# Kernel optimization log

Hardware: AMD Instinct MI355X
Metric: run time of the kernel (lower is better)

## Reference

```python
import jax, jax.numpy as jnp
import numpy as np

B_, L_ = 8, 2048            # batch, seq_len
AD, VD, H = 512, 512, 256    # audio_dim, visual_dim, hidden_dim (= mamba d_model)
EXPAND, DSTATE, DCONV = 2, 16, 4
DIN = EXPAND * H             # mamba d_inner = 512
DTRANK = (H + 15) // 16      # ceil(d_model/16) = 16
NCLS = 8


def setup_inputs() -> dict:
    key = jax.random.key(0)
    ks = jax.random.split(key, 16)
    w = lambda k, shape, s=0.02: jax.random.normal(k, shape, jnp.float32) * s
    return {
        "audio_feats": jax.random.normal(ks[0], (B_, L_, AD), jnp.float32),
        "visual_feats": jax.random.normal(ks[1], (B_, L_, VD), jnp.float32),
        "audio_w": w(ks[2], (H, AD)), "audio_b": jnp.zeros((H,), jnp.float32),
        "visual_w": w(ks[3], (H, VD)), "visual_b": jnp.zeros((H,), jnp.float32),
        "q_w": w(ks[4], (H, H)), "q_b": jnp.zeros((H,), jnp.float32),
        "k_w": w(ks[5], (H, H)), "k_b": jnp.zeros((H,), jnp.float32),
        "v_w": w(ks[6], (H, H)), "v_b": jnp.zeros((H,), jnp.float32),
        "in_proj_w": w(ks[7], (2 * DIN, H)),
        "conv_w": w(ks[8], (DIN, DCONV), 0.1), "conv_b": jnp.zeros((DIN,), jnp.float32),
        "x_proj_w": w(ks[9], (DTRANK + 2 * DSTATE, DIN)),
        "dt_proj_w": w(ks[10], (DIN, DTRANK), 0.1),
        "dt_proj_b": jnp.full((DIN,), -4.0, jnp.float32),  # softplus(-4) ~ small dt
        "A_log": jnp.log(jnp.tile(jnp.arange(1, DSTATE + 1, dtype=jnp.float32), (DIN, 1))),
        "D": jnp.ones((DIN,), jnp.float32),
        "out_proj_w": w(ks[11], (H, DIN)),
        "cls_w": w(ks[12], (NCLS, H)), "cls_b": jnp.zeros((NCLS,), jnp.float32),
    }


def _linear(x, w, b):
    return jnp.einsum('...i,oi->...o', x, w) + b


def _mamba(u, in_proj_w, conv_w, conv_b, x_proj_w, dt_proj_w, dt_proj_b, A_log, D, out_proj_w):
    # u: [B, L, d_model]
    xz = jnp.einsum('bld,ed->ble', u, in_proj_w)          # [B, L, 2*DIN]
    x, z = jnp.split(xz, 2, axis=-1)
    # causal depthwise conv1d (torch pads d_conv-1 both sides then truncates to L)
    lhs = jnp.swapaxes(x, 1, 2)                            # [B, DIN, L]
    rhs = conv_w[:, None, :]                               # [DIN, 1, DCONV]
    xc = jax.lax.conv_general_dilated(lhs, rhs, (1,), [(DCONV - 1, 0)],
                                      feature_group_count=DIN)
    x = jax.nn.silu(jnp.swapaxes(xc, 1, 2) + conv_b)       # [B, L, DIN]
    dbc = jnp.einsum('bld,ed->ble', x, x_proj_w)           # [B, L, DTRANK+2*DSTATE]
    dt, Bm, Cm = jnp.split(dbc, [DTRANK, DTRANK + DSTATE], axis=-1)
    dt = jax.nn.softplus(jnp.einsum('blr,dr->bld', dt, dt_proj_w) + dt_proj_b)
    A = -jnp.exp(A_log)                                    # [DIN, DSTATE]

    def step(h, inputs):
        dt_t, B_t, C_t, x_t = inputs                       # [B,DIN],[B,DSTATE],[B,DSTATE],[B,DIN]
        dA = jnp.exp(dt_t[:, :, None] * A)                 # [B, DIN, DSTATE]
        h = dA * h + (dt_t * x_t)[:, :, None] * B_t[:, None, :]
        y = jnp.einsum('bds,bs->bd', h, C_t)
        return h, y

    h0 = jnp.zeros((u.shape[0], DIN, DSTATE), x.dtype)
    xs = (jnp.swapaxes(dt, 0, 1), jnp.swapaxes(Bm, 0, 1),
          jnp.swapaxes(Cm, 0, 1), jnp.swapaxes(x, 0, 1))
    _, ys = jax.lax.scan(step, h0, xs)                     # ys: [L, B, DIN]
    y = jnp.swapaxes(ys, 0, 1) + x * D
    y = y * jax.nn.silu(z)
    return jnp.einsum('bld,od->blo', y, out_proj_w)        # [B, L, d_model]


def reference(audio_feats, visual_feats, audio_w, audio_b, visual_w, visual_b,
              q_w, q_b, k_w, k_b, v_w, v_b, in_proj_w, conv_w, conv_b,
              x_proj_w, dt_proj_w, dt_proj_b, A_log, D, out_proj_w, cls_w, cls_b):
    ah = _linear(audio_feats, audio_w, audio_b)            # [B, L, H]
    vh = _linear(visual_feats, visual_w, visual_b)         # [B, L, H]
    Q = _linear(ah, q_w, q_b)
    K = _linear(vh, k_w, k_b)
    V = _linear(vh, v_w, v_b)
    scores = jnp.einsum('bqd,bkd->bqk', Q, K) / jnp.sqrt(jnp.float32(H))
    attn = jax.nn.softmax(scores, axis=-1)                 # [B, L, L]
    fused = jnp.einsum('bqk,bkd->bqd', attn, V)            # [B, L, H]
    mo = _mamba(fused, in_proj_w, conv_w, conv_b, x_proj_w,
                dt_proj_w, dt_proj_b, A_log, D, out_proj_w)
    pooled = mo.mean(axis=1)                               # [B, H]
    logits = _linear(pooled, cls_w, cls_b)                 # [B, NCLS]
    preds = jax.nn.softmax(logits, axis=-1)
    return logits, preds
```

## Files before the change

kernel.cpp:

```cpp
#include <hip/hip_runtime.h>
#include <hip/hip_bf16.h>
#include <math.h>

#define B_    8
#define L_    2048
#define AD    512
#define VD    512
#define H_    256
#define DIN   512
#define DSTATE 16
#define DCONV  4
#define DTRANK 16
#define NCLS   8
#define BL    (B_ * L_)
#define NCH   64
#define CLEN  32
#define NSP   4
#define NGRP  8

typedef __attribute__((ext_vector_type(8))) short bf16x8;
typedef __attribute__((ext_vector_type(4))) float f32x4;

__device__ inline bf16x8 pack8(float4 a, float4 b)
{
    bf16x8 o; __hip_bfloat16 t;
    t = __float2bfloat16(a.x); o[0] = *(short*)&t;
    t = __float2bfloat16(a.y); o[1] = *(short*)&t;
    t = __float2bfloat16(a.z); o[2] = *(short*)&t;
    t = __float2bfloat16(a.w); o[3] = *(short*)&t;
    t = __float2bfloat16(b.x); o[4] = *(short*)&t;
    t = __float2bfloat16(b.y); o[5] = *(short*)&t;
    t = __float2bfloat16(b.z); o[6] = *(short*)&t;
    t = __float2bfloat16(b.w); o[7] = *(short*)&t;
    return o;
}

__device__ __forceinline__ void gload_lds16(const void* g, void* l)
{
    __builtin_amdgcn_global_load_lds(
        (const __attribute__((address_space(1))) void*)g,
        (__attribute__((address_space(3))) void*)l,
        16, 0, 0);
}

__global__ __launch_bounds__(256)
void cast_inputs_kernel(const float* __restrict__ a, const float* __restrict__ v,
                        __hip_bfloat16* __restrict__ ab, __hip_bfloat16* __restrict__ vb)
{
    size_t i = ((size_t)blockIdx.x * 256 + threadIdx.x) * 8;
    const float* s; __hip_bfloat16* d; size_t off;
    if (i < 8388608) { s = a; d = ab; off = i; }
    else             { s = v; d = vb; off = i - 8388608; }
    float4 x = *(const float4*)(s + off);
    float4 y = *(const float4*)(s + off + 4);
    *(bf16x8*)(d + off) = pack8(x, y);
}

__global__ __launch_bounds__(256)
void prep_kernel(const float* __restrict__ qw, const float* __restrict__ kw,
                 const float* __restrict__ vw, const float* __restrict__ ipw,
                 const float* __restrict__ xpw,
                 const float* __restrict__ aw, const float* __restrict__ vww,
                 const float* __restrict__ ab, const float* __restrict__ vb,
                 const float* __restrict__ qb, const float* __restrict__ kb,
                 const float* __restrict__ vb2,
                 __hip_bfloat16* __restrict__ qwb, __hip_bfloat16* __restrict__ kwb,
                 __hip_bfloat16* __restrict__ vwb, __hip_bfloat16* __restrict__ ipwb,
                 __hip_bfloat16* __restrict__ xpwb,
                 __hip_bfloat16* __restrict__ awT, __hip_bfloat16* __restrict__ vwT,
                 float* __restrict__ bq, float* __restrict__ bkv)
{
    const int blk = blockIdx.x;
    if (blk < 236) {
        size_t i = ((size_t)blk * 256 + threadIdx.x) * 8;
        const float* s; __hip_bfloat16* d; size_t off;
        if      (i <  65536) { s = qw;  d = qwb;  off = i; }
        else if (i < 131072) { s = kw;  d = kwb;  off = i - 65536; }
        else if (i < 196608) { s = vw;  d = vwb;  off = i - 131072; }
        else if (i < 458752) { s = ipw; d = ipwb; off = i - 196608; }
        else                 { s = xpw; d = xpwb; off = i - 458752; }
        float4 x = *(const float4*)(s + off);
        float4 y = *(const float4*)(s + off + 4);
        *(bf16x8*)(d + off) = pack8(x, y);
    } else if (blk < 1260) {
        int i = (blk - 236) * 256 + threadIdx.x;
        const float* s = (i < 131072) ? aw : vww;
        __hip_bfloat16* d = (i < 131072) ? awT : vwT;
        int j = i & 131071;
        int r = j >> 9, c = j & 511;
        d[c * 256 + r] = __float2bfloat16(s[j]);
    } else {
        int seg = blk - 1260;
        int m = threadIdx.x;
        const float* w  = (seg == 0) ? qw : (seg == 1) ? kw : vw;
        const float* ib = (seg == 0) ? ab : vb;
        const float* ob = (seg == 0) ? qb : (seg == 1) ? kb : vb2;
        float s = ob[m];
        for (int i = 0; i < 256; ++i) s += w[m * 256 + i] * ib[i];
        if (seg == 0) bq[m] = s;
        else          bkv[(seg - 1) * 256 + m] = s;
    }
}

__global__ __launch_bounds__(64, 2)
void gemm_comp_kernel(const __hip_bfloat16* __restrict__ qw,
                      const __hip_bfloat16* __restrict__ kw,
                      const __hip_bfloat16* __restrict__ vw,
                      const __hip_bfloat16* __restrict__ awT,
                      const __hip_bfloat16* __restrict__ vwT,
                      __hip_bfloat16* __restrict__ Wqp,
                      __hip_bfloat16* __restrict__ Wkvp)
{
    const int seg = blockIdx.z;
    const __hip_bfloat16* A = (seg == 0) ? qw : (seg == 1) ? kw : vw;
    const __hip_bfloat16* W = (seg == 0) ? awT : vwT;
    __hip_bfloat16* outp = (seg == 0) ? Wqp : (Wkvp + (size_t)(seg - 1) * 256 * 512);

    const int lane = threadIdx.x;
    const int l15  = lane & 15;
    const int quad = lane >> 4;
    const int m0   = blockIdx.x * 16;
    const int n0   = blockIdx.y * 64;

    const __hip_bfloat16* Arow = A + (size_t)(m0 + l15) * 256 + quad * 8;
    f32x4 acc[4];
    #pragma unroll
    for (int nt = 0; nt < 4; ++nt) acc[nt] = (f32x4){0.f, 0.f, 0.f, 0.f};

    #pragma unroll
    for (int kc = 0; kc < 256; kc += 32) {
        bf16x8 af = *(const bf16x8*)(Arow + kc);
        #pragma unroll
        for (int nt = 0; nt < 4; ++nt) {
            bf16x8 bfv = *(const bf16x8*)(W + (size_t)(n0 + nt * 16 + l15) * 256 + kc + quad * 8);
            acc[nt] = __builtin_amdgcn_mfma_f32_16x16x32_bf16(af, bfv, acc[nt], 0, 0, 0);
        }
    }
    #pragma unroll
    for (int nt = 0; nt < 4; ++nt) {
        int col = n0 + nt * 16 + l15;
        #pragma unroll
        for (int r = 0; r < 4; ++r)
            outp[(size_t)(m0 + quad * 4 + r) * 512 + col] = __float2bfloat16(acc[nt][r]);
    }
}

template<int N, int K, int NT, int OBF, int ACT>
__global__ __launch_bounds__(256, 2)
void gemm4_t(const __hip_bfloat16* __restrict__ A,
             const __hip_bfloat16* __restrict__ W,
             const float* __restrict__ bias,
             void* __restrict__ outp)
{
    constexpr int NROWS = NT * 16;
    __shared__ __attribute__((aligned(16))) short Ws[NROWS * 264];
    const int tid  = threadIdx.x;
    const int lane = tid & 63;
    const int w    = tid >> 6;
    const int l15  = lane & 15;
    const int quad = lane >> 4;
    const int m0   = blockIdx.x * 64 + w * 16;
    const int n0   = blockIdx.y * 64;

    constexpr int KC = K / 32;
    bf16x8 af[KC];
    const __hip_bfloat16* Arow = A + (size_t)(m0 + l15) * K + quad * 8;
    #pragma unroll
    for (int kc = 0; kc < KC; ++kc) af[kc] = *(const bf16x8*)(Arow + kc * 32);

    f32x4 acc[NT];
    #pragma unroll
    for (int nt = 0; nt < NT; ++nt) acc[nt] = (f32x4){0.f, 0.f, 0.f, 0.f};

    #pragma unroll
    for (int kh = 0; kh < K / 256; ++kh) {
        __syncthreads();
        #pragma unroll
        for (int i = 0; i < 8; ++i) {
            int id = tid + i * 256;
            int row = id >> 5, c = id & 31;
            if (row < NROWS)
                *(bf16x8*)&Ws[row * 264 + c * 8] =
                    *(const bf16x8*)(W + (size_t)(n0 + row) * K + kh * 256 + c * 8);
        }
        __syncthreads();
        #pragma unroll
        for (int kc = 0; kc < 8; ++kc) {
            #pragma unroll
            for (int nt = 0; nt < NT; ++nt) {
                bf16x8 wv = *(const bf16x8*)&Ws[(nt * 16 + l15) * 264 + kc * 32 + quad * 8];
                acc[nt] = __builtin_amdgcn_mfma_f32_16x16x32_bf16(af[kh * 8 + kc], wv, acc[nt], 0, 0, 0);
            }
        }
    }
    #pragma unroll
    for (int nt = 0; nt < NT; ++nt) {
        int col = n0 + nt * 16 + l15;
        float bv = bias ? bias[col] : 0.f;
        #pragma unroll
        for (int r = 0; r < 4; ++r) {
            size_t idx = (size_t)(m0 + quad * 4 + r) * N + col;
            float v = acc[nt][r] + bv;
            if (ACT) v = v / (1.f + __expf(-v));
            if (OBF) ((__hip_bfloat16*)outp)[idx] = __float2bfloat16(v);
            else     ((float*)outp)[idx] = v;
        }
    }
}

__global__ __launch_bounds__(256)
void transpose_v_kernel(const __hip_bfloat16* __restrict__ KV,
                        __hip_bfloat16* __restrict__ Vt)
{
    const int tid = threadIdx.x;
    const int lc  = blockIdx.x & 7;
    const int hg  = (blockIdx.x >> 3) & 31;
    const int b   = blockIdx.x >> 8;
    const int l   = lc * 256 + tid;
    bf16x8 v = *(const bf16x8*)(KV + ((size_t)b * L_ + l) * 512 + 256 + hg * 8);
    __hip_bfloat16* dst = Vt + (size_t)b * H_ * L_ + (size_t)(hg * 8) * L_ + l;
    #pragma unroll
    for (int j = 0; j < 8; ++j) {
        short s = v[j];
        dst[(size_t)j * L_] = *(__hip_bfloat16*)&s;
    }
}

__global__ __launch_bounds__(256, 2)
void attn_split_kernel(const __hip_bfloat16* __restrict__ Q,
                       const __hip_bfloat16* __restrict__ KV,
                       const __hip_bfloat16* __restrict__ Vt,
                       __hip_bfloat16* __restrict__ Opart,
                       float* __restrict__ lpart)
{
    __shared__ __attribute__((aligned(16))) short Ks[2][32 * 256];
    __shared__ __attribute__((aligned(16))) short Vs[2][256 * 32];
    __shared__ __attribute__((aligned(16))) short Pls[4][2][16 * 40];

    const int tid  = threadIdx.x;
    const int lane = tid & 63;
    const int w    = tid >> 6;
    const int b    = blockIdx.x & 7;
    const int qt   = (blockIdx.x >> 3) & 15;
    const int sp   = blockIdx.x >> 7;
    const int q0   = qt * 128 + w * 32;
    const int l15  = lane & 15;
    const int quad = lane >> 4;
    const int wb   = tid & 192;

    const __hip_bfloat16* Qb = Q  + ((size_t)b * L_ + q0) * H_;
    const __hip_bfloat16* Kb = KV + (size_t)b * L_ * 512;
    const __hip_bfloat16* Vb = Vt + (size_t)b * H_ * L_;

    bf16x8 qf[2][8];
    #pragma unroll
    for (int s2 = 0; s2 < 2; ++s2)
        #pragma unroll
        for (int kc = 0; kc < 8; ++kc)
            qf[s2][kc] = *(const bf16x8*)(Qb + (size_t)(s2 * 16 + l15) * H_ + kc * 32 + quad * 8);

    f32x4 Oacc[2][16];
    #pragma unroll
    for (int s2 = 0; s2 < 2; ++s2)
        #pragma unroll
        for (int nt = 0; nt < 16; ++nt) Oacc[s2][nt] = (f32x4){0.f, 0.f, 0.f, 0.f};
    float lsum[2][4] = {{0.f,0.f,0.f,0.f},{0.f,0.f,0.f,0.f}};

    const int kbase = sp * 512;
    const int sK = l15 & 7;
    const int vcol8 = (quad ^ (l15 & 3)) * 8;

#define STAGE(KsD, VsD, stv) do {                                                 \
        const int kb_ = kbase + (stv) * 32;                                       \
        _Pragma("unroll")                                                         \
        for (int i_ = 0; i_ < 4; ++i_) {                                          \
            int q_ = i_ * 256 + tid;                                              \
            int rK_ = q_ >> 5, cK_ = q_ & 31;                                     \
            gload_lds16(Kb + (size_t)(kb_ + rK_) * 512 + ((cK_ ^ (rK_ & 7)) << 3),\
                        (KsD) + (i_ * 256 + wb) * 8);                             \
            int rV_ = q_ >> 2, cV_ = q_ & 3;                                      \
            gload_lds16(Vb + (size_t)rV_ * L_ + kb_ + ((cV_ ^ (rV_ & 3)) << 3),   \
                        (VsD) + (i_ * 256 + wb) * 8);                             \
        }                                                                         \
    } while (0)

    STAGE(Ks[0], Vs[0], 0);
    __syncthreads();
    for (int st = 0; st < 16; ++st) {
        const int cur = st & 1;
        short* KsC = Ks[cur];
        short* VsC = Vs[cur];
        if (st < 15) STAGE(Ks[cur ^ 1], Vs[cur ^ 1], st + 1);
        #pragma unroll
        for (int nt = 0; nt < 2; ++nt) {
            f32x4 S0 = (f32x4){0.f,0.f,0.f,0.f};
            f32x4 S1 = (f32x4){0.f,0.f,0.f,0.f};
            __builtin_amdgcn_s_setprio(1);
            #pragma unroll
            for (int kc = 0; kc < 8; ++kc) {
                bf16x8 bk = *(const bf16x8*)&KsC[(nt * 16 + l15) * 256 + (((kc * 4 + quad) ^ sK) << 3)];
                S0 = __builtin_amdgcn_mfma_f32_16x16x32_bf16(qf[0][kc], bk, S0, 0, 0, 0);
                S1 = __builtin_amdgcn_mfma_f32_16x16x32_bf16(qf[1][kc], bk, S1, 0, 0, 0);
            }
            __builtin_amdgcn_s_setprio(0);
            #pragma unroll
            for (int r = 0; r < 4; ++r) {
                float p0 = __expf(S0[r] * 0.0625f);
                float p1 = __expf(S1[r] * 0.0625f);
                lsum[0][r] += p0;
                lsum[1][r] += p1;
                __hip_bfloat16 pb0 = __float2bfloat16(p0);
                __hip_bfloat16 pb1 = __float2bfloat16(p1);
                Pls[w][0][(quad * 4 + r) * 40 + nt * 16 + l15] = *(short*)&pb0;
                Pls[w][1][(quad * 4 + r) * 40 + nt * 16 + l15] = *(short*)&pb1;
            }
        }
        bf16x8 pf0 = *(const bf16x8*)&Pls[w][0][l15 * 40 + quad * 8];
        bf16x8 pf1 = *(const bf16x8*)&Pls[w][1][l15 * 40 + quad * 8];
        __builtin_amdgcn_s_setprio(1);
        #pragma unroll
        for (int nt = 0; nt < 16; ++nt) {
            bf16x8 vf = *(const bf16x8*)&VsC[(nt * 16 + l15) * 32 + vcol8];
            Oacc[0][nt] = __builtin_amdgcn_mfma_f32_16x16x32_bf16(pf0, vf, Oacc[0][nt], 0, 0, 0);
            Oacc[1][nt] = __builtin_amdgcn_mfma_f32_16x16x32_bf16(pf1, vf, Oacc[1][nt], 0, 0, 0);
        }
        __builtin_amdgcn_s_setprio(0);
        __syncthreads();
    }
#undef STAGE
    #pragma unroll
    for (int s2 = 0; s2 < 2; ++s2)
        #pragma unroll
        for (int r = 0; r < 4; ++r) {
            lsum[s2][r] += __shfl_xor(lsum[s2][r], 1, 64);
            lsum[s2][r] += __shfl_xor(lsum[s2][r], 2, 64);
            lsum[s2][r] += __shfl_xor(lsum[s2][r], 4, 64);
            lsum[s2][r] += __shfl_xor(lsum[s2][r], 8, 64);
        }
    __hip_bfloat16* Ob = Opart + (((size_t)sp * B_ + b) * L_ + q0) * H_;
    #pragma unroll
    for (int s2 = 0; s2 < 2; ++s2)
        #pragma unroll
        for (int r = 0; r < 4; ++r)
            #pragma unroll
            for (int nt = 0; nt < 16; ++nt)
                Ob[(size_t)(s2 * 16 + quad * 4 + r) * H_ + nt * 16 + l15] =
                    __float2bfloat16(Oacc[s2][nt][r]);
    if (l15 == 0) {
        #pragma unroll
        for (int s2 = 0; s2 < 2; ++s2)
            #pragma unroll
            for (int r = 0; r < 4; ++r)
                lpart[((size_t)sp * B_ + b) * L_ + q0 + s2 * 16 + quad * 4 + r] = lsum[s2][r];
    }
}

__global__ __launch_bounds__(256)
void attn_merge_kernel(const __hip_bfloat16* __restrict__ Opart,
                       const float* __restrict__ lpart,
                       __hip_bfloat16* __restrict__ O)
{
    const size_t i8  = ((size_t)blockIdx.x * 256 + threadIdx.x) * 8;
    const size_t row = i8 >> 8;
    float l = 0.f;
    #pragma unroll
    for (int sp = 0; sp < NSP; ++sp) l += lpart[(size_t)sp * BL + row];
    const float inv = 1.f / l;
    float o[8] = {0.f,0.f,0.f,0.f,0.f,0.f,0.f,0.f};
    #pragma unroll
    for (int sp = 0; sp < NSP; ++sp) {
        bf16x8 v = *(const bf16x8*)(Opart + (size_t)sp * BL * H_ + i8);
        #pragma unroll
        for (int j = 0; j < 8; ++j) {
            short s = v[j];
            o[j] += __bfloat162float(*(__hip_bfloat16*)&s);
        }
    }
    bf16x8 ov;
    #pragma unroll
    for (int j = 0; j < 8; ++j) {
        __hip_bfloat16 t = __float2bfloat16(o[j] * inv);
        ov[j] = *(short*)&t;
    }
    *(bf16x8*)(O + i8) = ov;
}

__global__ __launch_bounds__(256)
void conv_silu_kernel(const __hip_bfloat16* __restrict__ xb,
                      const float* __restrict__ cw,
                      const float* __restrict__ cb,
                      __hip_bfloat16* __restrict__ xconvbf)
{
    const int idx = blockIdx.x * 256 + threadIdx.x;
    const int d0 = (idx & 63) << 3;
    const int l  = (idx >> 6) & (L_ - 1);
    const int b  = idx >> 17;

    float4 wv[8];
    float acc[8];
    #pragma unroll
    for (int j = 0; j < 8; ++j) {
        wv[j]  = *(const float4*)(cw + (d0 + j) * DCONV);
        acc[j] = cb[d0 + j];
    }
    #pragma unroll
    for (int t = 0; t < DCONV; ++t) {
        int ls = l - (DCONV - 1) + t;
        if (ls >= 0) {
            bf16x8 x = *(const bf16x8*)(xb + ((size_t)b * L_ + ls) * DIN + d0);
            #pragma unroll
            for (int j = 0; j < 8; ++j) {
                short s = x[j];
                float xv = __bfloat162float(*(__hip_bfloat16*)&s);
                float wt = (t == 0) ? wv[j].x : (t == 1) ? wv[j].y : (t == 2) ? wv[j].z : wv[j].w;
                acc[j] += xv * wt;
            }
        }
    }
    bf16x8 ov;
    #pragma unroll
    for (int j = 0; j < 8; ++j) {
        float v = acc[j] / (1.f + __expf(-acc[j]));
        __hip_bfloat16 t = __float2bfloat16(v);
        ov[j] = *(short*)&t;
    }
    *(bf16x8*)(xconvbf + (size_t)idx * 8) = ov;
}

__global__ __launch_bounds__(256)
void scan_p1_kernel(const __hip_bfloat16* __restrict__ xconv,
                    const __hip_bfloat16* __restrict__ zw,
                    const float* __restrict__ dbc,
                    const float* __restrict__ dtw,
                    const float* __restrict__ dtbias,
                    const float* __restrict__ A_log,
                    const float* __restrict__ Dv,
                    float* __restrict__ hend,
                    float* __restrict__ aprod,
                    float* __restrict__ Gbuf,
                    float* __restrict__ accloc)
{
    __shared__ float Ds[CLEN][16];
    __shared__ float Bs[CLEN][16];
    __shared__ float Cs[CLEN][16];
    const int tid  = threadIdx.x;
    const int dgrp = blockIdx.x & 1;
    const int c    = (blockIdx.x >> 1) & 63;
    const int b    = blockIdx.x >> 7;
    const int d    = dgrp * 256 + tid;
    const size_t rbase = (size_t)b * L_ + c * CLEN;

    for (int i = tid; i < CLEN * 16; i += 256) {
        int tl = i >> 4, s = i & 15;
        Ds[tl][s] = dbc[(rbase + tl) * 48 + s];
        Bs[tl][s] = dbc[(rbase + tl) * 48 + 16 + s];
        Cs[tl][s] = dbc[(rbase + tl) * 48 + 32 + s];
    }
    __syncthreads();

    float wr[16];
    #pragma unroll
    for (int r = 0; r < 16; ++r) wr[r] = dtw[d * DTRANK + r];
    const float dbias = dtbias[d];
    const float Dval  = Dv[d];

    float Aa[16];
    bool fast = true;
    #pragma unroll
    for (int s = 0; s < 16; ++s) {
        Aa[s] = -__expf(A_log[d * DSTATE + s]);
        fast = fast && (fabsf(Aa[s] + (float)(s + 1)) < 1e-3f);
    }

    float h[16], ap[16], g[16];
    #pragma unroll
    for (int s = 0; s < 16; ++s) { h[s] = 0.f; ap[s] = 1.f; g[s] = 0.f; }
    float acc = 0.f;

    if (fast) {
        for (int t = 0; t < CLEN; ++t) {
            float d0 = dbias, d1 = 0.f;
            #pragma unroll
            for (int r = 0; r < 8; ++r) { d0 += Ds[t][r] * wr[r]; d1 += Ds[t][r + 8] * wr[r + 8]; }
            float dot = d0 + d1;
            float dtv = (dot > 20.f) ? dot : __logf(1.f + __expf(dot));
            float xv  = __bfloat162float(xconv[(rbase + t) * DIN + d]);
            float wt  = __bfloat162float(zw   [(rbase + t) * DIN + d]);
            float u  = dtv * xv;
            float e1 = __expf(-dtv);
            float ep = 1.f;
            #pragma unroll
            for (int s = 0; s < 16; ++s) {
                ep *= e1;
                ap[s] *= ep;
                h[s] = ep * h[s] + u * Bs[t][s];
                float tc = wt * Cs[t][s];
                acc += tc * h[s];
                g[s] += tc * ap[s];
            }
            acc += wt * xv * Dval;
        }
    } else {
        for (int t = 0; t < CLEN; ++t) {
            float d0 = dbias, d1 = 0.f;
            #pragma unroll
            for (int r = 0; r < 8; ++r) { d0 += Ds[t][r] * wr[r]; d1 += Ds[t][r + 8] * wr[r + 8]; }
            float dot = d0 + d1;
            float dtv = (dot > 20.f) ? dot : __logf(1.f + __expf(dot));
            float xv  = __bfloat162float(xconv[(rbase + t) * DIN + d]);
            float wt  = __bfloat162float(zw   [(rbase + t) * DIN + d]);
            float u  = dtv * xv;
            #pragma unroll
            for (int s = 0; s < 16; ++s) {
                float e = __expf(dtv * Aa[s]);
                ap[s] *= e;
                h[s] = e * h[s] + u * Bs[t][s];
                float tc = wt * Cs[t][s];
                acc += tc * h[s];
                g[s] += tc * ap[s];
            }
            acc += wt * xv * Dval;
        }
    }
    size_t o = (((size_t)b * NCH + c) * DIN + d) * 16;
    #pragma unroll
    for (int s = 0; s < 16; ++s) { hend[o + s] = h[s]; aprod[o + s] = ap[s]; Gbuf[o + s] = g[s]; }
    accloc[((size_t)b * NCH + c) * DIN + d] = acc;
}

__global__ __launch_bounds__(256)
void scan_p2a_kernel(const float* __restrict__ hend,
                     const float* __restrict__ aprod,
                     const float* __restrict__ Gbuf,
                     const float* __restrict__ accloc,
                     float* __restrict__ hg, float* __restrict__ Pg,
                     float* __restrict__ Wg, float* __restrict__ part0g,
                     float* __restrict__ accg)
{
    const int g   = blockIdx.x * 256 + threadIdx.x;
    const int b   = g >> 16;
    const int grp = (g >> 13) & 7;
    const int ds  = g & 8191;
    float h = 0.f, P = 1.f, W = 0.f, p0 = 0.f;
    #pragma unroll
    for (int j = 0; j < 8; ++j) {
        int c = grp * 8 + j;
        size_t idx = (((size_t)b * NCH + c) << 13) + ds;
        float G = Gbuf[idx], ap = aprod[idx], he = hend[idx];
        p0 += G * h;
        W  += G * P;
        h   = ap * h + he;
        P  *= ap;
    }
    size_t o = (((size_t)b * NGRP + grp) << 13) + ds;
    hg[o] = h; Pg[o] = P; Wg[o] = W; part0g[o] = p0;
    if (ds < DIN) {
        float a = 0.f;
        #pragma unroll
        for (int j = 0; j < 8; ++j)
            a += accloc[((size_t)b * NCH + grp * 8 + j) * DIN + ds];
        accg[((size_t)b * NGRP + grp) * DIN + ds] = a;
    }
}

__global__ __launch_bounds__(256)
void scan_p2b_kernel(const float* __restrict__ hg, const float* __restrict__ Pg,
                     const float* __restrict__ Wg, const float* __restrict__ part0g,
                     const float* __restrict__ accg,
                     float* __restrict__ ybar)
{
    const int g  = blockIdx.x * 256 + threadIdx.x;
    const int b  = g >> 13;
    const int ds = g & 8191;
    const int d  = ds >> 4;
    const int s  = ds & 15;
    float h = 0.f, part = 0.f;
    #pragma unroll
    for (int grp = 0; grp < NGRP; ++grp) {
        size_t o = (((size_t)b * NGRP + grp) << 13) + ds;
        part += part0g[o] + Wg[o] * h;
        h = Pg[o] * h + hg[o];
    }
    part += __shfl_xor(part, 1, 64);
    part += __shfl_xor(part, 2, 64);
    part += __shfl_xor(part, 4, 64);
    part += __shfl_xor(part, 8, 64);
    if (s == 0) {
        float a = 0.f;
        #pragma unroll
        for (int grp = 0; grp < NGRP; ++grp)
            a += accg[((size_t)b * NGRP + grp) * DIN + d];
        ybar[b * DIN + d] = (part + a) * (1.f / (float)L_);
    }
}

__global__ __launch_bounds__(256)
void head_kernel(const float* __restrict__ ybar,
                 const float* __restrict__ opw,
                 const float* __restrict__ clsw,
                 const float* __restrict__ clsb,
                 float* __restrict__ out)
{
    __shared__ float pooled_s[H_];
    __shared__ float logit_s[NCLS];
    const int tid = threadIdx.x;
    const int b   = blockIdx.x;
    const float* yb = ybar + b * DIN;
    const float* wr = opw + (size_t)tid * DIN;
    float p = 0.f;
    for (int dd = 0; dd < DIN; dd += 4) {
        float4 y4 = *(const float4*)(yb + dd);
        float4 w4 = *(const float4*)(wr + dd);
        p += y4.x*w4.x + y4.y*w4.y + y4.z*w4.z + y4.w*w4.w;
    }
    pooled_s[tid] = p;
    __syncthreads();
    if (tid < NCLS) {
        float lg = clsb[tid];
        const float* cw = clsw + tid * H_;
        for (int hh = 0; hh < H_; ++hh) lg += pooled_s[hh] * cw[hh];
        logit_s[tid] = lg;
        out[b * NCLS + tid] = lg;
    }
    __syncthreads();
    if (tid == 0) {
        float mx = logit_s[0];
        for (int c = 1; c < NCLS; ++c) mx = fmaxf(mx, logit_s[c]);
        float ssum = 0.f; float e[NCLS];
        for (int c = 0; c < NCLS; ++c) { e[c] = __expf(logit_s[c] - mx); ssum += e[c]; }
        for (int c = 0; c < NCLS; ++c) out[B_*NCLS + b * NCLS + c] = e[c] / ssum;
    }
}

extern "C" void kernel_launch(void* const* d_in, const int* in_sizes, int n_in,
                              void* d_out, int out_size, void* d_ws, size_t ws_size,
                              hipStream_t stream)
{
    const float* audio    = (const float*)d_in[0];
    const float* visual   = (const float*)d_in[1];
    const float* audio_w  = (const float*)d_in[2];
    const float* audio_b  = (const float*)d_in[3];
    const float* visual_w = (const float*)d_in[4];
    const float* visual_b = (const float*)d_in[5];
    const float* q_w = (const float*)d_in[6];
    const float* q_b = (const float*)d_in[7];
    const float* k_w = (const float*)d_in[8];
    const float* k_b = (const float*)d_in[9];
    const float* v_w = (const float*)d_in[10];
    const float* v_b = (const float*)d_in[11];
    const float* in_proj_w = (const float*)d_in[12];
    const float* conv_w    = (const float*)d_in[13];
    const float* conv_b    = (const float*)d_in[14];
    const float* x_proj_w  = (const float*)d_in[15];
    const float* dt_proj_w = (const float*)d_in[16];
    const float* dt_proj_b = (const float*)d_in[17];
    const float* A_log     = (const float*)d_in[18];
    const float* Dvec      = (const float*)d_in[19];
    const float* out_proj_w= (const float*)d_in[20];
    const float* cls_w     = (const float*)d_in[21];
    const float* cls_b     = (const float*)d_in[22];
    float* out = (float*)d_out;
    float* ws  = (float*)d_ws;

    __hip_bfloat16* abf  = (__hip_bfloat16*)(ws);
    __hip_bfloat16* vbf  = (__hip_bfloat16*)(ws + 4194304);
    __hip_bfloat16* Qbf  = (__hip_bfloat16*)(ws + 8388608);
    __hip_bfloat16* KVbf = (__hip_bfloat16*)(ws + 10485760);
    __hip_bfloat16* Vt   = (__hip_bfloat16*)(ws + 14680064);
    __hip_bfloat16* fusedbf = (__hip_bfloat16*)(ws + 16777216);
    __hip_bfloat16* Opart   = (__hip_bfloat16*)(ws + 18874368);
    __hip_bfloat16* xconvbf = (__hip_bfloat16*)(ws + 27262976);
    __hip_bfloat16* xbufbf = (__hip_bfloat16*)(ws);
    __hip_bfloat16* zwbf   = (__hip_bfloat16*)(ws + 4194304);
    float* hend   = ws;
    float* Gbuf   = ws + 18874368;
    float* aprod  = ws + 23068672;
    float* hg     = ws + 16777216;
    float* Pg     = ws + 17301504;
    float* Wgb    = ws + 17825792;
    float* part0g = ws + 18350080;
    __hip_bfloat16* q_wbf   = (__hip_bfloat16*)(ws + 31457280);
    __hip_bfloat16* k_wbf   = (__hip_bfloat16*)(ws + 31490048);
    __hip_bfloat16* v_wbf   = (__hip_bfloat16*)(ws + 31522816);
    __hip_bfloat16* ipwbf   = (__hip_bfloat16*)(ws + 31555584);
    __hip_bfloat16* xpwbf   = (__hip_bfloat16*)(ws + 31686656);
    __hip_bfloat16* awT     = (__hip_bfloat16*)(ws + 31698944);
    __hip_bfloat16* vwT     = (__hip_bfloat16*)(ws + 31764480);
    __hip_bfloat16* Wqp     = (__hip_bfloat16*)(ws + 31830016);
    __hip_bfloat16* Wkvp    = (__hip_bfloat16*)(ws + 31895552);
    float* bq     = ws + 32026624;
    float* bkv    = ws + 32026880;
    float* lpart  = ws + 32027392;
    float* dbcb   = ws + 32092928;
    float* accloc = ws + 32879360;
    float* accg   = ws + 33141504;
    float* ybar   = ws + 33174272;
    (void)ws_size;

    dim3 blk(256);
    cast_inputs_kernel<<<dim3(8192), blk, 0, stream>>>(audio, visual, abf, vbf);
    prep_kernel<<<dim3(1263), blk, 0, stream>>>(q_w, k_w, v_w, in_proj_w, x_proj_w,
                                                audio_w, visual_w, audio_b, visual_b,
                                                q_b, k_b, v_b,
                                                q_wbf, k_wbf, v_wbf, ipwbf, xpwbf,
                                                awT, vwT, bq, bkv);
    gemm_comp_kernel<<<dim3(16, 8, 3), dim3(64), 0, stream>>>(q_wbf, k_wbf, v_wbf, awT, vwT, Wqp, Wkvp);
    gemm4_t<256, 512, 4, 1, 0><<<dim3(256, 4), blk, 0, stream>>>(abf, Wqp,  bq,  Qbf);
    gemm4_t<512, 512, 4, 1, 0><<<dim3(256, 8), blk, 0, stream>>>(vbf, Wkvp, bkv, KVbf);
    transpose_v_kernel<<<dim3(2048), blk, 0, stream>>>(KVbf, Vt);
    attn_split_kernel<<<dim3(512), blk, 0, stream>>>(Qbf, KVbf, Vt, Opart, lpart);
    attn_merge_kernel<<<dim3(2048), blk, 0, stream>>>(Opart, lpart, fusedbf);
    gemm4_t<512, 256, 4, 1, 0><<<dim3(256, 8), blk, 0, stream>>>(fusedbf, ipwbf,           nullptr, xbufbf);
    gemm4_t<512, 256, 4, 1, 1><<<dim3(256, 8), blk, 0, stream>>>(fusedbf, ipwbf + DIN*H_,  nullptr, zwbf);
    conv_silu_kernel<<<dim3(4096), blk, 0, stream>>>(xbufbf, conv_w, conv_b, xconvbf);
    gemm4_t<48, 512, 3, 0, 0><<<dim3(256, 1), blk, 0, stream>>>(xconvbf, xpwbf, nullptr, dbcb);
    scan_p1_kernel<<<dim3(1024), blk, 0, stream>>>(xconvbf, zwbf, dbcb, dt_proj_w, dt_proj_b,
                                                   A_log, Dvec, hend, aprod, Gbuf, accloc);
    scan_p2a_kernel<<<dim3(2048), blk, 0, stream>>>(hend, aprod, Gbuf, accloc,
                                                    hg, Pg, Wgb, part0g, accg);
    scan_p2b_kernel<<<dim3(256), blk, 0, stream>>>(hg, Pg, Wgb, part0g, accg, ybar);
    head_kernel<<<dim3(8), blk, 0, stream>>>(ybar, out_proj_w, cls_w, cls_b, out);
}
```

Before: 428.1 us.

## Halve scan chunk length and recompute chunk decay from summed dt

```diff
diff --git a/kernel.cpp b/kernel.cpp
--- a/kernel.cpp
+++ b/kernel.cpp
@@ -13,8 +13,8 @@
 #define DTRANK 16
 #define NCLS   8
 #define BL    (B_ * L_)
-#define NCH   64
-#define CLEN  32
+#define NCH   128
+#define CLEN  16
 #define NSP   4
 #define NGRP  8
 
@@ -436,7 +436,7 @@
                     const float* __restrict__ A_log,
                     const float* __restrict__ Dv,
                     float* __restrict__ hend,
-                    float* __restrict__ aprod,
+                    float* __restrict__ sumdt,
                     float* __restrict__ Gbuf,
                     float* __restrict__ accloc)
 {
@@ -445,8 +445,8 @@
     __shared__ float Cs[CLEN][16];
     const int tid  = threadIdx.x;
     const int dgrp = blockIdx.x & 1;
-    const int c    = (blockIdx.x >> 1) & 63;
-    const int b    = blockIdx.x >> 7;
+    const int c    = (blockIdx.x >> 1) & (NCH - 1);
+    const int b    = blockIdx.x >> 8;
     const int d    = dgrp * 256 + tid;
     const size_t rbase = (size_t)b * L_ + c * CLEN;
 
@@ -476,6 +476,7 @@
     #pragma unroll
     for (int s = 0; s < 16; ++s) { h[s] = 0.f; ap[s] = 1.f; g[s] = 0.f; }
     float acc = 0.f;
+    float dts = 0.f;
 
     if (fast) {
         for (int t = 0; t < CLEN; ++t) {
@@ -489,6 +490,7 @@
             float u  = dtv * xv;
             float e1 = __expf(-dtv);
             float ep = 1.f;
+            dts += dtv;
             #pragma unroll
             for (int s = 0; s < 16; ++s) {
                 ep *= e1;
@@ -510,6 +512,7 @@
             float xv  = __bfloat162float(xconv[(rbase + t) * DIN + d]);
             float wt  = __bfloat162float(zw   [(rbase + t) * DIN + d]);
             float u  = dtv * xv;
+            dts += dtv;
             #pragma unroll
             for (int s = 0; s < 16; ++s) {
                 float e = __expf(dtv * Aa[s]);
@@ -524,15 +527,17 @@
     }
     size_t o = (((size_t)b * NCH + c) * DIN + d) * 16;
     #pragma unroll
-    for (int s = 0; s < 16; ++s) { hend[o + s] = h[s]; aprod[o + s] = ap[s]; Gbuf[o + s] = g[s]; }
+    for (int s = 0; s < 16; ++s) { hend[o + s] = h[s]; Gbuf[o + s] = g[s]; }
+    sumdt [((size_t)b * NCH + c) * DIN + d] = dts;
     accloc[((size_t)b * NCH + c) * DIN + d] = acc;
 }
 
 __global__ __launch_bounds__(256)
 void scan_p2a_kernel(const float* __restrict__ hend,
-                     const float* __restrict__ aprod,
+                     const float* __restrict__ sumdt,
                      const float* __restrict__ Gbuf,
                      const float* __restrict__ accloc,
+                     const float* __restrict__ A_log,
                      float* __restrict__ hg, float* __restrict__ Pg,
                      float* __restrict__ Wg, float* __restrict__ part0g,
                      float* __restrict__ accg)
@@ -541,12 +546,17 @@
     const int b   = g >> 16;
     const int grp = (g >> 13) & 7;
     const int ds  = g & 8191;
+    const int d   = ds >> 4;
+    const int s   = ds & 15;
+    const float Aa = -__expf(A_log[d * DSTATE + s]);
     float h = 0.f, P = 1.f, W = 0.f, p0 = 0.f;
     #pragma unroll
-    for (int j = 0; j < 8; ++j) {
-        int c = grp * 8 + j;
+    for (int j = 0; j < NCH / NGRP; ++j) {
+        int c = grp * (NCH / NGRP) + j;
         size_t idx = (((size_t)b * NCH + c) << 13) + ds;
-        float G = Gbuf[idx], ap = aprod[idx], he = hend[idx];
+        float G  = Gbuf[idx];
+        float he = hend[idx];
+        float ap = __expf(Aa * sumdt[((size_t)b * NCH + c) * DIN + d]);
         p0 += G * h;
         W  += G * P;
         h   = ap * h + he;
@@ -557,8 +567,8 @@
     if (ds < DIN) {
         float a = 0.f;
         #pragma unroll
-        for (int j = 0; j < 8; ++j)
-            a += accloc[((size_t)b * NCH + grp * 8 + j) * DIN + ds];
+        for (int j = 0; j < NCH / NGRP; ++j)
+            a += accloc[((size_t)b * NCH + grp * (NCH / NGRP) + j) * DIN + ds];
         accg[((size_t)b * NGRP + grp) * DIN + ds] = a;
     }
 }
@@ -672,9 +682,10 @@
     __hip_bfloat16* xconvbf = (__hip_bfloat16*)(ws + 27262976);
     __hip_bfloat16* xbufbf = (__hip_bfloat16*)(ws);
     __hip_bfloat16* zwbf   = (__hip_bfloat16*)(ws + 4194304);
-    float* hend   = ws;
+    float* sumdt  = ws;
+    float* accloc = ws + 524288;
+    float* hend   = ws + 8388608;
     float* Gbuf   = ws + 18874368;
-    float* aprod  = ws + 23068672;
     float* hg     = ws + 16777216;
     float* Pg     = ws + 17301504;
     float* Wgb    = ws + 17825792;
@@ -692,7 +703,6 @@
     float* bkv    = ws + 32026880;
     float* lpart  = ws + 32027392;
     float* dbcb   = ws + 32092928;
-    float* accloc = ws + 32879360;
     float* accg   = ws + 33141504;
     float* ybar   = ws + 33174272;
     (void)ws_size;
@@ -714,9 +724,9 @@
     gemm4_t<512, 256, 4, 1, 1><<<dim3(256, 8), blk, 0, stream>>>(fusedbf, ipwbf + DIN*H_,  nullptr, zwbf);
     conv_silu_kernel<<<dim3(4096), blk, 0, stream>>>(xbufbf, conv_w, conv_b, xconvbf);
     gemm4_t<48, 512, 3, 0, 0><<<dim3(256, 1), blk, 0, stream>>>(xconvbf, xpwbf, nullptr, dbcb);
-    scan_p1_kernel<<<dim3(1024), blk, 0, stream>>>(xconvbf, zwbf, dbcb, dt_proj_w, dt_proj_b,
-                                                   A_log, Dvec, hend, aprod, Gbuf, accloc);
-    scan_p2a_kernel<<<dim3(2048), blk, 0, stream>>>(hend, aprod, Gbuf, accloc,
+    scan_p1_kernel<<<dim3(2048), blk, 0, stream>>>(xconvbf, zwbf, dbcb, dt_proj_w, dt_proj_b,
+                                                   A_log, Dvec, hend, sumdt, Gbuf, accloc);
+    scan_p2a_kernel<<<dim3(2048), blk, 0, stream>>>(hend, sumdt, Gbuf, accloc, A_log,
                                                     hg, Pg, Wgb, part0g, accg);
     scan_p2b_kernel<<<dim3(256), blk, 0, stream>>>(hg, Pg, Wgb, part0g, accg, ybar);
     head_kernel<<<dim3(8), blk, 0, stream>>>(ybar, out_proj_w, cls_w, cls_b, out);
```

Result: no change. 423.4 us (-1.1%).
